# Kernel optimization log

Hardware: AMD Instinct MI355X
Metric: run time of the kernel (lower is better)

The kernel has to match this reference:

```python
import jax, jax.numpy as jnp
import numpy as np

WINDOW_SIZE = 11
SIGMA = 1.5
C1 = 0.01 ** 2
C2 = 0.03 ** 2


def _gaussian_window(window_size, sigma, channel):
    x = np.arange(window_size)
    g = np.exp(-((x - window_size // 2) ** 2) / (2.0 * sigma ** 2))
    g = g / g.sum()
    w2d = np.outer(g, g).astype(np.float32)  # [K,K]
    # depthwise kernel [C,1,K,K] (OIHW with feature_group_count=C)
    return jnp.asarray(np.broadcast_to(w2d, (channel, 1, window_size, window_size)))


def _depthwise_conv(x, window):
    # x: [B,C,H,W], window: [C,1,K,K]; SAME padding, groups=C
    pad = WINDOW_SIZE // 2
    return jax.lax.conv_general_dilated(
        x, window,
        window_strides=(1, 1),
        padding=[(pad, pad), (pad, pad)],
        dimension_numbers=('NCHW', 'OIHW', 'NCHW'),
        feature_group_count=x.shape[1],
    )


def setup_inputs() -> dict:
    key = jax.random.key(0)
    k1, k2 = jax.random.split(key)
    shape = (16, 3, 512, 512)
    img1 = jax.random.uniform(k1, shape, dtype=jnp.float32)
    img2 = jax.random.uniform(k2, shape, dtype=jnp.float32)
    return {"img1": img1, "img2": img2}


def reference(img1, img2):
    channel = img1.shape[1]
    window = _gaussian_window(WINDOW_SIZE, SIGMA, channel).astype(img1.dtype)

    mu1 = _depthwise_conv(img1, window)
    mu2 = _depthwise_conv(img2, window)
    mu1_sq = mu1 * mu1
    mu2_sq = mu2 * mu2
    mu1_mu2 = mu1 * mu2

    sigma1_sq = _depthwise_conv(img1 * img1, window) - mu1_sq
    sigma2_sq = _depthwise_conv(img2 * img2, window) - mu2_sq
    sigma12 = _depthwise_conv(img1 * img2, window) - mu1_mu2

    ssim_map = ((2 * mu1_mu2 + C1) * (2 * sigma12 + C2)) / (
        (mu1_sq + mu2_sq + C1) * (sigma1_sq + sigma2_sq + C2))
    # size_average=True -> scalar mean
    return jnp.mean(ssim_map)
```

## Files before the change

### kernel.cpp

```cpp
#include <hip/hip_runtime.h>

#define IMG 512
#define NPLANES 48
#define TW 64
#define TH 32
#define RD 5
#define KW 11
#define VC (TW + 2*RD)
#define WPAD 80
#define PRW (2*VC + 4)
#define NTX (IMG/TW)
#define NTY (IMG/TH)
#define TPP (NTX*NTY)
#define NBLOCKS (NPLANES*TPP)
#define NPIX (16.0f*3.0f*512.0f*512.0f)

typedef float v2f __attribute__((ext_vector_type(2)));

__device__ __forceinline__ v2f pk_fma(v2f a, v2f b, v2f c) {
    v2f d;
    asm("v_pk_fma_f32 %0, %1, %2, %3" : "=v"(d) : "v"(a), "v"(b), "v"(c));
    return d;
}
__device__ __forceinline__ v2f pk_mul(v2f a, v2f b) {
    v2f d;
    asm("v_pk_mul_f32 %0, %1, %2" : "=v"(d) : "v"(a), "v"(b));
    return d;
}

__device__ __forceinline__ float fast_rcp(float d) {
    float r = __builtin_amdgcn_rcpf(d);
    r = r * (2.0f - d * r);
    return r;
}

__global__ __launch_bounds__(256) void ssim_kernel(
    const float* __restrict__ img1, const float* __restrict__ img2,
    float* __restrict__ partial)
{
    __shared__ __align__(16) float v01[TH][PRW];
    __shared__ __align__(16) float v23[TH][PRW];
    __shared__ __align__(16) float vZ [TH][WPAD];
    __shared__ float wsum[4];

    const float cw[KW] = {
        0.00102838f, 0.00759876f, 0.03600077f, 0.10936069f, 0.21300553f,
        0.26601172f,
        0.21300553f, 0.10936069f, 0.03600077f, 0.00759876f, 0.00102838f
    };
    const v2f cw2[KW] = {
        {0.00102838f,0.00102838f}, {0.00759876f,0.00759876f},
        {0.03600077f,0.03600077f}, {0.10936069f,0.10936069f},
        {0.21300553f,0.21300553f}, {0.26601172f,0.26601172f},
        {0.21300553f,0.21300553f}, {0.10936069f,0.10936069f},
        {0.03600077f,0.03600077f}, {0.00759876f,0.00759876f},
        {0.00102838f,0.00102838f}
    };

    const int tid = threadIdx.x;
    const int blk = blockIdx.x;
    const int plane = blk / TPP;
    const int t     = blk % TPP;
    const int ty0 = (t / NTX) * TH;
    const int tx0 = (t % NTX) * TW;
    const float* __restrict__ p1 = img1 + (size_t)plane * IMG * IMG;
    const float* __restrict__ p2 = img2 + (size_t)plane * IMG * IMG;

    const bool interior = (tx0 >= RD) && (tx0 + TW + RD <= IMG) &&
                          (ty0 >= RD) && (ty0 + TH + RD <= IMG);

    for (int task = tid; task < VC * 4; task += 256) {
        const int col = task % VC;
        const int seg = task / VC;
        const int gx  = tx0 + col - RD;
        const int r0  = seg * 8;

        float a[18], b[18];
        if (interior) {
            const unsigned off0 = (unsigned)((ty0 + r0 - RD) * IMG + gx);
            #pragma unroll
            for (int k = 0; k < 18; k++) {
                a[k] = p1[off0 + (unsigned)(k * IMG)];
                b[k] = p2[off0 + (unsigned)(k * IMG)];
            }
        } else {
            const bool xok = (gx >= 0) && (gx < IMG);
            #pragma unroll
            for (int k = 0; k < 18; k++) {
                const int gy = ty0 + r0 + k - RD;
                const bool ok = xok && (gy >= 0) && (gy < IMG);
                const int gi = gy * IMG + gx;
                a[k] = ok ? p1[gi] : 0.f;
                b[k] = ok ? p2[gi] : 0.f;
            }
        }

        v2f sAB[8], sXY[8];
        float sZ[8];
        #pragma unroll
        for (int o = 0; o < 8; o++) {
            sAB[o] = (v2f){0.f, 0.f};
            sXY[o] = (v2f){0.f, 0.f};
            sZ[o]  = 0.f;
        }

        #pragma unroll
        for (int k = 0; k < 18; k++) {
            v2f rab; rab.x = a[k]; rab.y = b[k];
            const v2f rxy = pk_mul(rab, rab);
            const float ab = a[k] * b[k];
            #pragma unroll
            for (int o = 0; o < 8; o++) {
                const int d = k - o;
                if (d >= 0 && d < KW) {
                    sAB[o] = pk_fma(cw2[d], rab, sAB[o]);
                    sXY[o] = pk_fma(cw2[d], rxy, sXY[o]);
                    sZ[o]  = fmaf(cw[d], ab, sZ[o]);
                }
            }
        }

        #pragma unroll
        for (int o = 0; o < 8; o++) {
            const int r = r0 + o;
            *(v2f*)&v01[r][2*col] = sAB[o];
            *(v2f*)&v23[r][2*col] = sXY[o];
            vZ[r][col] = sZ[o];
        }
    }
    __syncthreads();

    const float C1 = 1e-4f;
    const float C2 = 9e-4f;
    const v2f NEG1 = {-1.f, -1.f};
    float acc = 0.f;
    #pragma unroll
    for (int it = 0; it < 2; it++) {
        const int task = tid + it * 256;
        const int j = task & 15;
        const int r = task >> 4;

        v2f prAB[14], prXY[14];
        {
            const float4* rowp = (const float4*)&v01[r][0];
            #pragma unroll
            for (int i = 0; i < 7; i++) {
                const float4 q = rowp[2*j + i];
                prAB[2*i]   = (v2f){q.x, q.y};
                prAB[2*i+1] = (v2f){q.z, q.w};
            }
        }
        {
            const float4* rowp = (const float4*)&v23[r][0];
            #pragma unroll
            for (int i = 0; i < 7; i++) {
                const float4 q = rowp[2*j + i];
                prXY[2*i]   = (v2f){q.x, q.y};
                prXY[2*i+1] = (v2f){q.z, q.w};
            }
        }
        float zv[16];
        {
            const float4* rowp = (const float4*)&vZ[r][0];
            #pragma unroll
            for (int i = 0; i < 4; i++) {
                const float4 q = rowp[j + i];
                zv[4*i] = q.x; zv[4*i+1] = q.y; zv[4*i+2] = q.z; zv[4*i+3] = q.w;
            }
        }

        #pragma unroll
        for (int o = 0; o < 4; o++) {
            v2f M  = (v2f){0.f, 0.f};
            v2f X  = (v2f){0.f, 0.f};
            float z = 0.f;
            #pragma unroll
            for (int d = 0; d < KW; d++) {
                M = pk_fma(cw2[d], prAB[o + d], M);
                X = pk_fma(cw2[d], prXY[o + d], X);
                z = fmaf(cw[d], zv[o + d], z);
            }
            const v2f M2 = pk_mul(M, M);
            const v2f S  = pk_fma(M2, NEG1, X);
            const float mu12 = M.x * M.y;
            const float s12  = z - mu12;
            const float num = fmaf(2.f, mu12, C1) * fmaf(2.f, s12, C2);
            const float den = (M2.x + M2.y + C1) * (S.x + S.y + C2);
            acc += num * fast_rcp(den);
        }
    }

    #pragma unroll
    for (int off = 32; off > 0; off >>= 1)
        acc += __shfl_down(acc, off, 64);
    const int lane = tid & 63;
    const int wv_i = tid >> 6;
    if (lane == 0) wsum[wv_i] = acc;
    __syncthreads();
    if (tid == 0)
        partial[blk] = (wsum[0] + wsum[1]) + (wsum[2] + wsum[3]);
}

__global__ __launch_bounds__(256) void ssim_reduce_kernel(
    const float* __restrict__ partial, float* __restrict__ out)
{
    float acc = 0.f;
    for (int i = threadIdx.x; i < NBLOCKS; i += 256)
        acc += partial[i];
    #pragma unroll
    for (int off = 32; off > 0; off >>= 1)
        acc += __shfl_down(acc, off, 64);
    __shared__ float wsum[4];
    const int lane = threadIdx.x & 63;
    const int wv_i = threadIdx.x >> 6;
    if (lane == 0) wsum[wv_i] = acc;
    __syncthreads();
    if (threadIdx.x == 0)
        out[0] = ((wsum[0] + wsum[1]) + (wsum[2] + wsum[3])) * (1.0f / NPIX);
}

extern "C" void kernel_launch(void* const* d_in, const int* in_sizes, int n_in,
                              void* d_out, int out_size, void* d_ws, size_t ws_size,
                              hipStream_t stream) {
    const float* img1 = (const float*)d_in[0];
    const float* img2 = (const float*)d_in[1];
    float* out = (float*)d_out;
    float* partial = (float*)d_ws;

    ssim_kernel<<<NBLOCKS, 256, 0, stream>>>(img1, img2, partial);
    ssim_reduce_kernel<<<1, 256, 0, stream>>>(partial, out);
}
```

Baseline: 156.6 us.

## Convolve sum/difference images to cut five blurred fields to four

Rewrites the SSIM statistics in terms of s=a+b and d=a-b, so only blur(s), blur(d), blur(s²) and blur(d²) are needed. The cross term and individual variances are recovered algebraically: 4*mu1*mu2 = mu_s² - mu_d², and mu1²+mu2² = (mu_s²+mu_d²)/2. This removes the scalar third channel from both the vertical and horizontal passes and the vZ shared buffer, lowering FMA count and LDS traffic. The cost is slightly different floating-point rounding from the cancellation in differences of squares.

Result: faster. 146.7 us (-6.3%).

```diff
diff --git a/kernel.cpp b/kernel.cpp
--- a/kernel.cpp
+++ b/kernel.cpp
@@ -7,8 +7,7 @@
 #define RD 5
 #define KW 11
 #define VC (TW + 2*RD)
-#define WPAD 80
-#define PRW (2*VC + 4)
+#define PRW (2*VC)
 #define NTX (IMG/TW)
 #define NTY (IMG/TH)
 #define TPP (NTX*NTY)
@@ -27,6 +26,12 @@
     asm("v_pk_mul_f32 %0, %1, %2" : "=v"(d) : "v"(a), "v"(b));
     return d;
 }
+__device__ __forceinline__ v2f pk_sd(float a, float b) {
+    v2f d;
+    d.x = a + b;
+    d.y = a - b;
+    return d;
+}
 
 __device__ __forceinline__ float fast_rcp(float d) {
     float r = __builtin_amdgcn_rcpf(d);
@@ -38,16 +43,10 @@
     const float* __restrict__ img1, const float* __restrict__ img2,
     float* __restrict__ partial)
 {
-    __shared__ __align__(16) float v01[TH][PRW];
-    __shared__ __align__(16) float v23[TH][PRW];
-    __shared__ __align__(16) float vZ [TH][WPAD];
+    __shared__ __align__(16) float vSD[TH][PRW];
+    __shared__ __align__(16) float vQ [TH][PRW];
     __shared__ float wsum[4];
 
-    const float cw[KW] = {
-        0.00102838f, 0.00759876f, 0.03600077f, 0.10936069f, 0.21300553f,
-        0.26601172f,
-        0.21300553f, 0.10936069f, 0.03600077f, 0.00759876f, 0.00102838f
-    };
     const v2f cw2[KW] = {
         {0.00102838f,0.00102838f}, {0.00759876f,0.00759876f},
         {0.03600077f,0.03600077f}, {0.10936069f,0.10936069f},
@@ -95,27 +94,20 @@
             }
         }
 
-        v2f sAB[8], sXY[8];
-        float sZ[8];
-        #pragma unroll
-        for (int o = 0; o < 8; o++) {
-            sAB[o] = (v2f){0.f, 0.f};
-            sXY[o] = (v2f){0.f, 0.f};
-            sZ[o]  = 0.f;
-        }
-
+        v2f sSD[8], sQ[8];
         #pragma unroll
         for (int k = 0; k < 18; k++) {
-            v2f rab; rab.x = a[k]; rab.y = b[k];
-            const v2f rxy = pk_mul(rab, rab);
-            const float ab = a[k] * b[k];
+            const v2f sd = pk_sd(a[k], b[k]);
+            const v2f q  = pk_mul(sd, sd);
             #pragma unroll
             for (int o = 0; o < 8; o++) {
                 const int d = k - o;
-                if (d >= 0 && d < KW) {
-                    sAB[o] = pk_fma(cw2[d], rab, sAB[o]);
-                    sXY[o] = pk_fma(cw2[d], rxy, sXY[o]);
-                    sZ[o]  = fmaf(cw[d], ab, sZ[o]);
+                if (d == 0) {
+                    sSD[o] = pk_mul(cw2[0], sd);
+                    sQ[o]  = pk_mul(cw2[0], q);
+                } else if (d > 0 && d < KW) {
+                    sSD[o] = pk_fma(cw2[d], sd, sSD[o]);
+                    sQ[o]  = pk_fma(cw2[d], q,  sQ[o]);
                 }
             }
         }
@@ -123,9 +115,8 @@
         #pragma unroll
         for (int o = 0; o < 8; o++) {
             const int r = r0 + o;
-            *(v2f*)&v01[r][2*col] = sAB[o];
-            *(v2f*)&v23[r][2*col] = sXY[o];
-            vZ[r][col] = sZ[o];
+            *(v2f*)&vSD[r][2 * col] = sSD[o];
+            *(v2f*)&vQ [r][2 * col] = sQ[o];
         }
     }
     __syncthreads();
@@ -140,52 +131,43 @@
         const int j = task & 15;
         const int r = task >> 4;
 
-        v2f prAB[14], prXY[14];
+        v2f prSD[14], prQ[14];
         {
-            const float4* rowp = (const float4*)&v01[r][0];
+            const float4* rowp = (const float4*)&vSD[r][0];
             #pragma unroll
             for (int i = 0; i < 7; i++) {
-                const float4 q = rowp[2*j + i];
-                prAB[2*i]   = (v2f){q.x, q.y};
-                prAB[2*i+1] = (v2f){q.z, q.w};
+                const float4 q = rowp[2 * j + i];
+                prSD[2 * i]     = (v2f){q.x, q.y};
+                prSD[2 * i + 1] = (v2f){q.z, q.w};
             }
         }
         {
-            const float4* rowp = (const float4*)&v23[r][0];
+            const float4* rowp = (const float4*)&vQ[r][0];
             #pragma unroll
             for (int i = 0; i < 7; i++) {
-                const float4 q = rowp[2*j + i];
-                prXY[2*i]   = (v2f){q.x, q.y};
-                prXY[2*i+1] = (v2f){q.z, q.w};
-            }
-        }
-        float zv[16];
-        {
-            const float4* rowp = (const float4*)&vZ[r][0];
-            #pragma unroll
-            for (int i = 0; i < 4; i++) {
-                const float4 q = rowp[j + i];
-                zv[4*i] = q.x; zv[4*i+1] = q.y; zv[4*i+2] = q.z; zv[4*i+3] = q.w;
+                const float4 q = rowp[2 * j + i];
+                prQ[2 * i]     = (v2f){q.x, q.y};
+                prQ[2 * i + 1] = (v2f){q.z, q.w};
             }
         }
 
         #pragma unroll
         for (int o = 0; o < 4; o++) {
-            v2f M  = (v2f){0.f, 0.f};
-            v2f X  = (v2f){0.f, 0.f};
-            float z = 0.f;
-            #pragma unroll
-            for (int d = 0; d < KW; d++) {
-                M = pk_fma(cw2[d], prAB[o + d], M);
-                X = pk_fma(cw2[d], prXY[o + d], X);
-                z = fmaf(cw[d], zv[o + d], z);
+            v2f M = pk_mul(cw2[0], prSD[o]);
+            v2f X = pk_mul(cw2[0], prQ[o]);
+            #pragma unroll
+            for (int d = 1; d < KW; d++) {
+                M = pk_fma(cw2[d], prSD[o + d], M);
+                X = pk_fma(cw2[d], prQ[o + d], X);
             }
             const v2f M2 = pk_mul(M, M);
-            const v2f S  = pk_fma(M2, NEG1, X);
-            const float mu12 = M.x * M.y;
-            const float s12  = z - mu12;
-            const float num = fmaf(2.f, mu12, C1) * fmaf(2.f, s12, C2);
-            const float den = (M2.x + M2.y + C1) * (S.x + S.y + C2);
+            const v2f V  = pk_fma(M2, NEG1, X);
+            const float mm = M2.x - M2.y;
+            const float mp = M2.x + M2.y;
+            const float vm = V.x - V.y;
+            const float vp = V.x + V.y;
+            const float num = fmaf(0.5f, mm, C1) * fmaf(0.5f, vm, C2);
+            const float den = fmaf(0.5f, mp, C1) * fmaf(0.5f, vp, C2);
             acc += num * fast_rcp(den);
         }
     }
```
